# Kernel tuning notes

Measured on AMD Instinct MI355X. Metric: run time of the kernel, lower is better.

## Reference

```python
import jax, jax.numpy as jnp
import numpy as np

PI = np.pi

def rgb_to_lab(img):
    # img: [B,3,H,W] sRGB in [0,1]. Matches kornia.color.rgb_to_lab.
    lin = jnp.where(img > 0.04045, jnp.power((img + 0.055) / 1.055, 2.4), img / 12.92)
    r, g, b = lin[:, 0], lin[:, 1], lin[:, 2]
    x = 0.412453 * r + 0.357580 * g + 0.180423 * b
    y = 0.212671 * r + 0.715160 * g + 0.072169 * b
    z = 0.019334 * r + 0.119193 * g + 0.950227 * b
    # normalize by D65 white point
    xn = x / 0.95047
    yn = y
    zn = z / 1.08883
    def f(t):
        return jnp.where(t > 0.008856, jnp.power(jnp.maximum(t, 1e-8), 1.0 / 3.0), 7.787 * t + 4.0 / 29.0)
    fx, fy, fz = f(xn), f(yn), f(zn)
    L = 116.0 * fy - 16.0
    a = 500.0 * (fx - fy)
    bb = 200.0 * (fy - fz)
    return L, a, bb  # each [B,H,W]

def deltaE_ciede2000(L1, a1, b1, L2, a2, b2):
    # skimage.color.deltaE_ciede2000 with kL=kC=kH=1
    C1 = jnp.hypot(a1, b1)
    C2 = jnp.hypot(a2, b2)
    Cbar = 0.5 * (C1 + C2)
    c7 = Cbar ** 7
    G = 0.5 * (1.0 - jnp.sqrt(c7 / (c7 + 25.0 ** 7)))
    scale = 1.0 + G
    a1p = a1 * scale
    a2p = a2 * scale
    C1p = jnp.hypot(a1p, b1)
    C2p = jnp.hypot(a2p, b2)
    h1 = jnp.arctan2(b1, a1p); h1 = jnp.where(h1 < 0, h1 + 2 * PI, h1)
    h2 = jnp.arctan2(b2, a2p); h2 = jnp.where(h2 < 0, h2 + 2 * PI, h2)
    # lightness term
    Lbar = 0.5 * (L1 + L2)
    tmp = (Lbar - 50.0) ** 2
    SL = 1.0 + 0.015 * tmp / jnp.sqrt(20.0 + tmp)
    L_term = (L2 - L1) / SL
    # chroma term
    Cbarp = 0.5 * (C1p + C2p)
    SC = 1.0 + 0.045 * Cbarp
    C_term = (C2p - C1p) / SC
    # hue term
    h_diff = h2 - h1
    h_sum = h1 + h2
    CC = C1p * C2p
    dH = jnp.where(h_diff > PI, h_diff - 2 * PI, jnp.where(h_diff < -PI, h_diff + 2 * PI, h_diff))
    dH = jnp.where(CC == 0.0, 0.0, dH)
    dH_term = 2.0 * jnp.sqrt(CC) * jnp.sin(dH / 2.0)
    mask = (CC != 0.0) & (jnp.abs(h_diff) > PI)
    Hbar = jnp.where(mask & (h_sum < 2 * PI), h_sum + 2 * PI,
                     jnp.where(mask & (h_sum >= 2 * PI), h_sum - 2 * PI, h_sum))
    Hbar = jnp.where(CC == 0.0, h_sum * 2.0, Hbar)
    Hbar = 0.5 * Hbar
    T = (1.0 - 0.17 * jnp.cos(Hbar - PI / 6.0)
         + 0.24 * jnp.cos(2.0 * Hbar)
         + 0.32 * jnp.cos(3.0 * Hbar + PI / 30.0)
         - 0.20 * jnp.cos(4.0 * Hbar - 63.0 * PI / 180.0))
    SH = 1.0 + 0.015 * Cbarp * T
    H_term = dH_term / SH
    # rotation term
    c7p = Cbarp ** 7
    Rc = 2.0 * jnp.sqrt(c7p / (c7p + 25.0 ** 7))
    dtheta = (PI / 6.0) * jnp.exp(-(((Hbar * 180.0 / PI) - 275.0) / 25.0) ** 2)
    R_term = -jnp.sin(2.0 * dtheta) * Rc * C_term * H_term
    dE2 = L_term ** 2 + C_term ** 2 + H_term ** 2 + R_term
    return jnp.sqrt(jnp.maximum(dE2, 0.0))


def setup_inputs() -> dict:
    key = jax.random.key(0)
    k1, k2 = jax.random.split(key)
    img1 = jax.random.uniform(k1, (16, 3, 512, 512), dtype=jnp.float32)
    img2 = jax.random.uniform(k2, (16, 3, 512, 512), dtype=jnp.float32)
    return {"img1": img1, "img2": img2}


def reference(img1, img2):
    L1, a1, b1 = rgb_to_lab(img1)
    L2, a2, b2 = rgb_to_lab(img2)
    delE = deltaE_ciede2000(L1, a1, b1, L2, a2, b2)  # [B,H,W]
    return delE / 100.0
```

## Files before the change

### kernel.cpp

```cpp
#include <hip/hip_runtime.h>
#include <math.h>

#define PI_F      3.14159265358979323846f
#define TWO_PI_F  6.28318530717958647692f
#define INV_2PI_F 0.15915494309189533577f

typedef float v2 __attribute__((ext_vector_type(2)));

__device__ __forceinline__ float fsqrt(float x)  { return __builtin_amdgcn_sqrtf(x); }
__device__ __forceinline__ float frcp(float x)   { return __builtin_amdgcn_rcpf(x); }
__device__ __forceinline__ float frsq(float x)   { return __builtin_amdgcn_rsqf(x); }
__device__ __forceinline__ float fexp2(float x)  { return __builtin_amdgcn_exp2f(x); }
__device__ __forceinline__ float flog2(float x)  { return __builtin_amdgcn_logf(x); }
__device__ __forceinline__ float fsin(float x)   { return __builtin_amdgcn_sinf(x * INV_2PI_F); }
__device__ __forceinline__ float fcos(float x)   { return __builtin_amdgcn_cosf(x * INV_2PI_F); }

__device__ __forceinline__ v2 V(float s){ v2 r; r.x = s; r.y = s; return r; }
__device__ __forceinline__ v2 V2(float a, float b){ v2 r; r.x = a; r.y = b; return r; }
#if __has_builtin(__builtin_elementwise_fma)
__device__ __forceinline__ v2 vfma(v2 a, v2 b, v2 c){ return __builtin_elementwise_fma(a, b, c); }
#else
__device__ __forceinline__ v2 vfma(v2 a, v2 b, v2 c){ v2 r; r.x=__fmaf_rn(a.x,b.x,c.x); r.y=__fmaf_rn(a.y,b.y,c.y); return r; }
#endif
__device__ __forceinline__ v2 vmax0(v2 a){ v2 r; r.x=fmaxf(a.x,0.0f); r.y=fmaxf(a.y,0.0f); return r; }
__device__ __forceinline__ v2 vsqrt(v2 x){ v2 r; r.x=fsqrt(x.x); r.y=fsqrt(x.y); return r; }
__device__ __forceinline__ v2 vrcp (v2 x){ v2 r; r.x=frcp(x.x);  r.y=frcp(x.y);  return r; }
__device__ __forceinline__ v2 vrsq (v2 x){ v2 r; r.x=frsq(x.x);  r.y=frsq(x.y);  return r; }
__device__ __forceinline__ v2 vexp2(v2 x){ v2 r; r.x=fexp2(x.x); r.y=fexp2(x.y); return r; }
__device__ __forceinline__ v2 vsinr(v2 x){ v2 r; r.x=fsin(x.x); r.y=fsin(x.y); return r; }
__device__ __forceinline__ v2 vcosr(v2 x){ v2 r; r.x=fcos(x.x); r.y=fcos(x.y); return r; }


__device__ __forceinline__ v2 vatan2(v2 y, v2 x) {
    v2 ax, ay; ax.x = fabsf(x.x); ax.y = fabsf(x.y); ay.x = fabsf(y.x); ay.y = fabsf(y.y);
    v2 mx, mn;
    mx.x = fmaxf(ax.x, ay.x); mx.y = fmaxf(ax.y, ay.y);
    mn.x = fminf(ax.x, ay.x); mn.y = fminf(ax.y, ay.y);
    v2 r = mn * vrcp(mx);
    v2 s = r * r;
    v2 p = vfma(s, V(-0.01172120f), V(0.05265332f));
    p = vfma(s, p, V(-0.11643287f));
    p = vfma(s, p, V( 0.19354346f));
    p = vfma(s, p, V(-0.33262347f));
    p = vfma(s, p, V( 0.99997726f));
    v2 th = r * p;
    th.x = (ay.x > ax.x)   ? (1.57079632679f - th.x) : th.x;
    th.y = (ay.y > ax.y)   ? (1.57079632679f - th.y) : th.y;
    th.x = (x.x < 0.0f)    ? (PI_F - th.x)           : th.x;
    th.y = (x.y < 0.0f)    ? (PI_F - th.y)           : th.y;
    th.x = (y.x < 0.0f)    ? -th.x                   : th.x;
    th.y = (y.y < 0.0f)    ? -th.y                   : th.y;
    th.x = (mx.x == 0.0f)  ? 0.0f                    : th.x;
    th.y = (mx.y == 0.0f)  ? 0.0f                    : th.y;
    return th;
}

__device__ __forceinline__ v2 vsrgb_lin(v2 c) {
    v2 u = vfma(c, V(1.0f / 1.055f), V(0.055f / 1.055f));
    v2 p; p.x = fexp2(2.4f * flog2(u.x)); p.y = fexp2(2.4f * flog2(u.y));
    v2 l = c * (1.0f / 12.92f);
    v2 r;
    r.x = (c.x > 0.04045f) ? p.x : l.x;
    r.y = (c.y > 0.04045f) ? p.y : l.y;
    return r;
}

__device__ __forceinline__ v2 vlabf(v2 t) {
    v2 cr; cr.x = fexp2(0.333333333333f * flog2(t.x)); cr.y = fexp2(0.333333333333f * flog2(t.y));
    v2 ln = vfma(V(7.787f), t, V(4.0f / 29.0f));
    v2 r;
    r.x = (t.x > 0.008856f) ? cr.x : ln.x;
    r.y = (t.y > 0.008856f) ? cr.y : ln.y;
    return r;
}

__device__ __forceinline__ void vrgb2lab(v2 r, v2 g, v2 b,
                                         v2& L, v2& A, v2& B) {
    r = vsrgb_lin(r); g = vsrgb_lin(g); b = vsrgb_lin(b);
    v2 xn = 0.4339463f * r + 0.3762135f * g + 0.1898252f * b;
    v2 yn = 0.212671f  * r + 0.71516f   * g + 0.072169f  * b;
    v2 zn = 0.0177566f * r + 0.1094694f * g + 0.8727056f * b;
    v2 fx = vlabf(xn);
    v2 fy = vlabf(yn);
    v2 fz = vlabf(zn);
    L = vfma(V(116.0f), fy, V(-16.0f));
    A = 500.0f * (fx - fy);
    B = 200.0f * (fy - fz);
}

__device__ __forceinline__ void hue_tail(float h1, float h2, float C1p, float C2p,
                                         float& dHt, float& Hb) {
    float h_diff = h2 - h1;
    float h_sum  = h1 + h2;
    float CC = C1p * C2p;
    bool cc0 = (CC == 0.0f);

    float dH = (h_diff > PI_F) ? (h_diff - TWO_PI_F)
             : ((h_diff < -PI_F) ? (h_diff + TWO_PI_F) : h_diff);
    if (cc0) dH = 0.0f;
    dHt = 2.0f * fsqrt(CC) * fsin(0.5f * dH);

    bool mask = (!cc0) && (fabsf(h_diff) > PI_F);
    float Hbar = h_sum;
    if (mask) Hbar = (h_sum < TWO_PI_F) ? (h_sum + TWO_PI_F) : (h_sum - TWO_PI_F);
    if (cc0)  Hbar = h_sum * 2.0f;
    Hb = 0.5f * Hbar;
}


__device__ __forceinline__ v2 chain_v2(v2 r1, v2 g1, v2 bl1,
                                       v2 r2, v2 g2, v2 bl2) {
    v2 L1, A1, B1, L2, A2, B2;
    vrgb2lab(r1, g1, bl1, L1, A1, B1);
    vrgb2lab(r2, g2, bl2, L2, A2, B2);

    const float P25_7 = 6103515625.0f;

    v2 C1 = vsqrt(vfma(A1, A1, B1 * B1));
    v2 C2 = vsqrt(vfma(A2, A2, B2 * B2));
    v2 Cbar = 0.5f * (C1 + C2);
    v2 cb2 = Cbar * Cbar;
    v2 c7 = cb2 * cb2 * cb2 * Cbar;
    v2 G = vfma(-0.5f * c7, vrsq(vfma(c7, c7, vfma(V(P25_7), c7, V(1e-20f)))), V(0.5f));
    v2 s = V(1.0f) + G;
    v2 a1p = A1 * s, a2p = A2 * s;
    v2 C1p = vsqrt(vfma(a1p, a1p, B1 * B1));
    v2 C2p = vsqrt(vfma(a2p, a2p, B2 * B2));

    v2 h1 = vatan2(B1, a1p);
    h1.x = (h1.x < 0.0f) ? h1.x + TWO_PI_F : h1.x;
    h1.y = (h1.y < 0.0f) ? h1.y + TWO_PI_F : h1.y;
    v2 h2 = vatan2(B2, a2p);
    h2.x = (h2.x < 0.0f) ? h2.x + TWO_PI_F : h2.x;
    h2.y = (h2.y < 0.0f) ? h2.y + TWO_PI_F : h2.y;

    v2 dHt, Hb;
    {
        float d0, b0, d1, b1v;
        hue_tail(h1.x, h2.x, C1p.x, C2p.x, d0, b0);
        hue_tail(h1.y, h2.y, C1p.y, C2p.y, d1, b1v);
        dHt.x = d0; dHt.y = d1; Hb.x = b0; Hb.y = b1v;
    }

    v2 Lbar = (L1 + L2) * 0.5f;
    v2 lt = Lbar - V(50.0f);
    v2 tmp = lt * lt;
    v2 SL = vfma(tmp * 0.015f, vrsq(V(20.0f) + tmp), V(1.0f));

    v2 Cbarp = (C1p + C2p) * 0.5f;
    v2 SC = vfma(V(0.045f), Cbarp, V(1.0f));

    v2 ch = vcosr(Hb);
    v2 sh = vsinr(Hb);
    v2 c2 = vfma(ch * 2.0f, ch, V(-1.0f));
    v2 s2 = sh * ch * 2.0f;
    v2 c3 = ch * c2 - sh * s2;
    v2 s3 = sh * c2 + ch * s2;
    v2 c4 = vfma(c2 * 2.0f, c2, V(-1.0f));
    v2 s4 = s2 * c2 * 2.0f;
    v2 T1 = vfma(ch, V(0.86602540378f), sh * 0.5f);
    v2 T3 = vfma(c3, V(0.99452189536f), s3 * -0.10452846327f);
    v2 T4 = vfma(c4, V(0.45399049974f), s4 * 0.89100652419f);
    v2 T = V(1.0f) - T1 * 0.17f + c2 * 0.24f + T3 * 0.32f - T4 * 0.20f;
    v2 SH = vfma(Cbarp * 0.015f, T, V(1.0f));

    v2 PQ  = SC * SH;
    v2 inv = vrcp(SL * PQ);
    v2 L_term = (L2 - L1) * PQ * inv;
    v2 C_term = (C2p - C1p) * (SL * SH) * inv;
    v2 H_term = dHt * (SL * SC) * inv;

    v2 cp2 = Cbarp * Cbarp;
    v2 c7p = cp2 * cp2 * cp2 * Cbarp;
    v2 Rc = c7p * 2.0f * vrsq(vfma(c7p, c7p, vfma(V(P25_7), c7p, V(1e-20f))));

    v2 hd = vfma(Hb, V(2.752769787f), V(-13.2123465f));
    v2 vv = vexp2(-(hd * hd)) * 1.04719755119f;
    v2 w  = vv * vv;
    v2 sp = vfma(w, V(-1.0f / 5040.0f), V(1.0f / 120.0f));
    sp = vfma(w, sp, V(-1.0f / 6.0f));
    sp = vfma(w, sp, V(1.0f));
    v2 sin2dt = vv * sp;
    v2 R_term = -(sin2dt * Rc * C_term * H_term);

    v2 dE2 = vfma(L_term, L_term, vfma(C_term, C_term, vfma(H_term, H_term, R_term)));
    return vsqrt(vmax0(dE2)) * 0.01f;
}


__global__ __launch_bounds__(256) void ciede_kernel(
    const float* __restrict__ img1, const float* __restrict__ img2,
    float* __restrict__ out, int n2_total) {
    int idx = blockIdx.x * 256 + threadIdx.x;
    if (idx >= n2_total) return;

    const int PLANE2 = 131072;
    int n = idx >> 17;
    int j = idx & (PLANE2 - 1);

    const float2* p1 = reinterpret_cast<const float2*>(img1) + (size_t)n * 3 * PLANE2;
    const float2* p2 = reinterpret_cast<const float2*>(img2) + (size_t)n * 3 * PLANE2;

    float2 r1 = p1[j], g1 = p1[j + PLANE2], b1 = p1[j + 2 * PLANE2];
    float2 r2 = p2[j], g2 = p2[j + PLANE2], b2 = p2[j + 2 * PLANE2];

    v2 o = chain_v2(V2(r1.x, r1.y), V2(g1.x, g1.y), V2(b1.x, b1.y),
                    V2(r2.x, r2.y), V2(g2.x, g2.y), V2(b2.x, b2.y));

    float2 ov; ov.x = o.x; ov.y = o.y;
    reinterpret_cast<float2*>(out)[idx] = ov;
}

extern "C" void kernel_launch(void* const* d_in, const int* in_sizes, int n_in,
                              void* d_out, int out_size, void* d_ws, size_t ws_size,
                              hipStream_t stream) {
    const float* img1 = (const float*)d_in[0];
    const float* img2 = (const float*)d_in[1];
    float* out = (float*)d_out;

    int n2 = out_size / 2;
    int grid = (n2 + 255) / 256;
    ciede_kernel<<<grid, 256, 0, stream>>>(img1, img2, out, n2);
}
```

Baseline: 128.0 us.

## Process four pixel pairs per thread with software-prefetched loads

Each thread now handles four strided element pairs, loading the next pair's six channels while computing the current one, and the grid is fixed at 2048 blocks. The goal is to overlap global memory latency with the heavy ALU chain and to cut the block count. It hardcodes the problem size (stride 524288, four iterations) and drops the bounds check. It also raises register pressure from holding two sets of inputs.

```diff
diff --git a/kernel.cpp b/kernel.cpp
--- a/kernel.cpp
+++ b/kernel.cpp
@@ -191,24 +191,44 @@
 __global__ __launch_bounds__(256) void ciede_kernel(
     const float* __restrict__ img1, const float* __restrict__ img2,
     float* __restrict__ out, int n2_total) {
-    int idx = blockIdx.x * 256 + threadIdx.x;
-    if (idx >= n2_total) return;
-
     const int PLANE2 = 131072;
-    int n = idx >> 17;
-    int j = idx & (PLANE2 - 1);
-
-    const float2* p1 = reinterpret_cast<const float2*>(img1) + (size_t)n * 3 * PLANE2;
-    const float2* p2 = reinterpret_cast<const float2*>(img2) + (size_t)n * 3 * PLANE2;
-
-    float2 r1 = p1[j], g1 = p1[j + PLANE2], b1 = p1[j + 2 * PLANE2];
-    float2 r2 = p2[j], g2 = p2[j + PLANE2], b2 = p2[j + 2 * PLANE2];
-
-    v2 o = chain_v2(V2(r1.x, r1.y), V2(g1.x, g1.y), V2(b1.x, b1.y),
-                    V2(r2.x, r2.y), V2(g2.x, g2.y), V2(b2.x, b2.y));
-
-    float2 ov; ov.x = o.x; ov.y = o.y;
-    reinterpret_cast<float2*>(out)[idx] = ov;
+    const int STRIDE = 524288;
+    int tid = blockIdx.x * 256 + threadIdx.x;
+
+    float2 r1a, g1a, b1a, r2a, g2a, b2a;
+    float2 r1b, g1b, b1b, r2b, g2b, b2b;
+
+    {
+        int idx = tid;
+        int n = idx >> 17;
+        int j = idx & (PLANE2 - 1);
+        const float2* p1 = reinterpret_cast<const float2*>(img1) + (size_t)n * 3 * PLANE2;
+        const float2* p2 = reinterpret_cast<const float2*>(img2) + (size_t)n * 3 * PLANE2;
+        r1a = p1[j]; g1a = p1[j + PLANE2]; b1a = p1[j + 2 * PLANE2];
+        r2a = p2[j]; g2a = p2[j + PLANE2]; b2a = p2[j + 2 * PLANE2];
+    }
+
+    #pragma unroll
+    for (int i = 0; i < 4; ++i) {
+        if (i < 3) {
+            int idx = tid + (i + 1) * STRIDE;
+            int n = idx >> 17;
+            int j = idx & (PLANE2 - 1);
+            const float2* p1 = reinterpret_cast<const float2*>(img1) + (size_t)n * 3 * PLANE2;
+            const float2* p2 = reinterpret_cast<const float2*>(img2) + (size_t)n * 3 * PLANE2;
+            r1b = p1[j]; g1b = p1[j + PLANE2]; b1b = p1[j + 2 * PLANE2];
+            r2b = p2[j]; g2b = p2[j + PLANE2]; b2b = p2[j + 2 * PLANE2];
+        }
+
+        v2 o = chain_v2(V2(r1a.x, r1a.y), V2(g1a.x, g1a.y), V2(b1a.x, b1a.y),
+                        V2(r2a.x, r2a.y), V2(g2a.x, g2a.y), V2(b2a.x, b2a.y));
+
+        float2 ov; ov.x = o.x; ov.y = o.y;
+        reinterpret_cast<float2*>(out)[tid + i * STRIDE] = ov;
+
+        r1a = r1b; g1a = g1b; b1a = b1b;
+        r2a = r2b; g2a = g2b; b2a = b2b;
+    }
 }
 
 extern "C" void kernel_launch(void* const* d_in, const int* in_sizes, int n_in,
@@ -219,6 +239,6 @@
     float* out = (float*)d_out;
 
     int n2 = out_size / 2;
-    int grid = (n2 + 255) / 256;
+    int grid = 2048;
     ciede_kernel<<<grid, 256, 0, stream>>>(img1, img2, out, n2);
 }
```

After: 132.2 us. +3.2%, slower.
